# Kernel tuning notes

Hardware: AMD Instinct MI355X
Metric: run time of the kernel (lower is better)

The kernel has to match this reference:

```python
import jax, jax.numpy as jnp
import numpy as np

# index_map: new group -> list of old column indices (covers 23 old classes -> 10 groups)
INDEX_MAP = {0: [0, 1], 1: [2, 3], 2: [4, 5, 6], 3: [7, 8], 4: [9, 10, 11],
             5: [12, 13], 6: [14, 15, 16], 7: [17, 18], 8: [19, 20], 9: [21, 22]}
C_OLD = 23
G = len(INDEX_MAP)

# Membership matrix M[c, g] = 1 if old column c belongs to group g.
# outputs[:, g] = sum_{c in group g} inputs[:, c]  ==  inputs @ M
_M_np = np.zeros((C_OLD, G), dtype=np.float32)
for g, olds in INDEX_MAP.items():
    for c in olds:
        _M_np[c, g] = 1.0

B, N = 8, 262144


def setup_inputs() -> dict:
    key = jax.random.key(0)
    k1, k2 = jax.random.split(key)
    inputs = jax.random.uniform(k1, (B, N, C_OLD), dtype=jnp.float32)  # positive logits/scores
    t = jax.random.uniform(k2, (B, G), dtype=jnp.float32)
    targets = t / jnp.sum(t, axis=-1, keepdims=True)  # probability targets for KLDiv
    return {"inputs": inputs, "targets": targets}


def reference(inputs, targets):
    M = jnp.asarray(_M_np)                                 # [C, G]
    # grouped scatter-sum over columns (the nested loops in the original)
    outputs = jnp.einsum('bnc,cg->bng', inputs, M)         # [B, N, G]
    probs = outputs / jnp.sum(outputs, axis=-1, keepdims=True)
    avg_probs = jnp.mean(probs, axis=1)                    # [B, G]
    log_avg = jnp.log(avg_probs)
    # KLDivLoss(reduction='batchmean') on a 1-D input of length G divides by G:
    # loss_b = sum_g t[g] * (log t[g] - log_avg[g]) / G
    kl_per_b = jnp.sum(targets * (jnp.log(targets) - log_avg), axis=-1) / G
    return jnp.mean(kl_per_b)
```

## Files before the change

### kernel.cpp

```cpp
#include <hip/hip_runtime.h>
#include <math.h>

#define C_OLD 23
#define G 10
#define BVAL 8
#define NVAL 262144
#define ROWS_PER_BLOCK 256
#define BLOCK 256
#define TILE_FLOATS (ROWS_PER_BLOCK * C_OLD)
#define TILE_VEC4   (TILE_FLOATS / 4)
#define FULL_VEC_ITERS (TILE_VEC4 / BLOCK)

__global__ void zero_ws_kernel(double* acc) {
    int t = threadIdx.x;
    if (t < BVAL * G) acc[t] = 0.0;
}

__global__ __launch_bounds__(BLOCK) void group_prob_sum_kernel(
        const float* __restrict__ in, double* __restrict__ acc) {
    __shared__ float tile[TILE_FLOATS];
    __shared__ float wpart[BLOCK / 64][G];

    const int tid = threadIdx.x;
    const long long row0 = (long long)blockIdx.x * ROWS_PER_BLOCK;

    const float4* __restrict__ src = (const float4*)(in + row0 * C_OLD);
    float4* dst = (float4*)tile;
    #pragma unroll
    for (int i = 0; i < FULL_VEC_ITERS; ++i)
        dst[tid + i * BLOCK] = src[tid + i * BLOCK];
    {
        int rem = tid + FULL_VEC_ITERS * BLOCK;
        if (rem < TILE_VEC4) dst[rem] = src[rem];
    }
    __syncthreads();

    const float* row = tile + tid * C_OLD;
    float s0 = row[0] + row[1];
    float s1 = row[2] + row[3];
    float s2 = row[4] + row[5] + row[6];
    float s3 = row[7] + row[8];
    float s4 = row[9] + row[10] + row[11];
    float s5 = row[12] + row[13];
    float s6 = row[14] + row[15] + row[16];
    float s7 = row[17] + row[18];
    float s8 = row[19] + row[20];
    float s9 = row[21] + row[22];
    float tot = ((s0 + s1) + (s2 + s3)) + ((s4 + s5) + (s6 + s7)) + (s8 + s9);
    float inv = 1.0f / tot;

    float p[G];
    p[0] = s0 * inv; p[1] = s1 * inv; p[2] = s2 * inv; p[3] = s3 * inv;
    p[4] = s4 * inv; p[5] = s5 * inv; p[6] = s6 * inv; p[7] = s7 * inv;
    p[8] = s8 * inv; p[9] = s9 * inv;

    #pragma unroll
    for (int g = 0; g < G; ++g) {
        float v = p[g];
        #pragma unroll
        for (int off = 32; off > 0; off >>= 1)
            v += __shfl_down(v, off, 64);
        p[g] = v;
    }

    const int wave = tid >> 6;
    const int lane = tid & 63;
    if (lane == 0) {
        #pragma unroll
        for (int g = 0; g < G; ++g) wpart[wave][g] = p[g];
    }
    __syncthreads();

    if (tid < G) {
        float sum = wpart[0][tid] + wpart[1][tid] + wpart[2][tid] + wpart[3][tid];
        const int b = (int)(row0 >> 18);
        atomicAdd(&acc[b * G + tid], (double)sum);
    }
}

__global__ void finalize_kernel(const double* __restrict__ acc,
                                const float* __restrict__ tgt,
                                float* __restrict__ out) {
    __shared__ double red[128];
    const int t = threadIdx.x;
    double term = 0.0;
    if (t < BVAL * G) {
        double avg = acc[t] / (double)NVAL;
        double tv = (double)tgt[t];
        term = tv * (log(tv) - log(avg));
    }
    red[t] = term;
    __syncthreads();
    #pragma unroll
    for (int s = 64; s > 0; s >>= 1) {
        if (t < s) red[t] += red[t + s];
        __syncthreads();
    }
    if (t == 0) out[0] = (float)(red[0] / (double)(G * BVAL));
}

extern "C" void kernel_launch(void* const* d_in, const int* in_sizes, int n_in,
                              void* d_out, int out_size, void* d_ws, size_t ws_size,
                              hipStream_t stream) {
    const float* inputs  = (const float*)d_in[0];
    const float* targets = (const float*)d_in[1];
    float* out = (float*)d_out;
    double* acc = (double*)d_ws;

    zero_ws_kernel<<<1, 128, 0, stream>>>(acc);

    const long long total_rows = (long long)BVAL * NVAL;
    const int nblocks = (int)(total_rows / ROWS_PER_BLOCK);
    group_prob_sum_kernel<<<nblocks, BLOCK, 0, stream>>>(inputs, acc);

    finalize_kernel<<<1, 128, 0, stream>>>(acc, targets, out);
}
```

Baseline: 283.5 us.

## Process multiple tiles per block and replace double atomics with partial-sum buffer

Each block now loops over 8 tiles of 256 rows, accumulating group probabilities in registers, and launches 1024 blocks instead of 8192. It writes per-block partial sums to workspace and lets the finalize kernel reduce them, which removes the zero kernel and all double-precision atomics. The goal is to cut atomic contention and per-block reduction overhead. In exchange the grid is much smaller, so there is less latency hiding: each tile load is serialized behind a sync with no overlap between loading and compute.

Result: faster. 270.0 us (-4.8%).

```diff
diff --git a/kernel.cpp b/kernel.cpp
--- a/kernel.cpp
+++ b/kernel.cpp
@@ -5,88 +5,94 @@
 #define G 10
 #define BVAL 8
 #define NVAL 262144
-#define ROWS_PER_BLOCK 256
 #define BLOCK 256
-#define TILE_FLOATS (ROWS_PER_BLOCK * C_OLD)
+#define ROWS_PER_TILE 256
+#define TILES 8
+#define BLOCKS_PER_B 128
+#define TILE_FLOATS (ROWS_PER_TILE * C_OLD)
 #define TILE_VEC4   (TILE_FLOATS / 4)
 #define FULL_VEC_ITERS (TILE_VEC4 / BLOCK)
 
-__global__ void zero_ws_kernel(double* acc) {
-    int t = threadIdx.x;
-    if (t < BVAL * G) acc[t] = 0.0;
-}
-
-__global__ __launch_bounds__(BLOCK) void group_prob_sum_kernel(
-        const float* __restrict__ in, double* __restrict__ acc) {
+__global__ __launch_bounds__(BLOCK) void group_prob_partial_kernel(
+        const float* __restrict__ in, float* __restrict__ part) {
     __shared__ float tile[TILE_FLOATS];
     __shared__ float wpart[BLOCK / 64][G];
 
     const int tid = threadIdx.x;
-    const long long row0 = (long long)blockIdx.x * ROWS_PER_BLOCK;
+    const int b   = blockIdx.x / BLOCKS_PER_B;
+    const int blk = blockIdx.x % BLOCKS_PER_B;
+    const long long rowBase = (long long)b * NVAL
+                            + (long long)blk * (ROWS_PER_TILE * TILES);
 
-    const float4* __restrict__ src = (const float4*)(in + row0 * C_OLD);
-    float4* dst = (float4*)tile;
+    float acc[G];
     #pragma unroll
-    for (int i = 0; i < FULL_VEC_ITERS; ++i)
-        dst[tid + i * BLOCK] = src[tid + i * BLOCK];
-    {
-        int rem = tid + FULL_VEC_ITERS * BLOCK;
-        if (rem < TILE_VEC4) dst[rem] = src[rem];
+    for (int g = 0; g < G; ++g) acc[g] = 0.0f;
+
+    for (int t = 0; t < TILES; ++t) {
+        const float4* __restrict__ src =
+            (const float4*)(in + (rowBase + (long long)t * ROWS_PER_TILE) * C_OLD);
+        float4* dst = (float4*)tile;
+        #pragma unroll
+        for (int i = 0; i < FULL_VEC_ITERS; ++i)
+            dst[tid + i * BLOCK] = src[tid + i * BLOCK];
+        if (tid < TILE_VEC4 - FULL_VEC_ITERS * BLOCK)
+            dst[tid + FULL_VEC_ITERS * BLOCK] = src[tid + FULL_VEC_ITERS * BLOCK];
+        __syncthreads();
+
+        const float* row = tile + tid * C_OLD;
+        float s0 = row[0] + row[1];
+        float s1 = row[2] + row[3];
+        float s2 = row[4] + row[5] + row[6];
+        float s3 = row[7] + row[8];
+        float s4 = row[9] + row[10] + row[11];
+        float s5 = row[12] + row[13];
+        float s6 = row[14] + row[15] + row[16];
+        float s7 = row[17] + row[18];
+        float s8 = row[19] + row[20];
+        float s9 = row[21] + row[22];
+        float tot = ((s0 + s1) + (s2 + s3)) + ((s4 + s5) + (s6 + s7)) + (s8 + s9);
+        float inv = 1.0f / tot;
+        acc[0] += s0 * inv; acc[1] += s1 * inv; acc[2] += s2 * inv;
+        acc[3] += s3 * inv; acc[4] += s4 * inv; acc[5] += s5 * inv;
+        acc[6] += s6 * inv; acc[7] += s7 * inv; acc[8] += s8 * inv;
+        acc[9] += s9 * inv;
+        __syncthreads();
     }
-    __syncthreads();
-
-    const float* row = tile + tid * C_OLD;
-    float s0 = row[0] + row[1];
-    float s1 = row[2] + row[3];
-    float s2 = row[4] + row[5] + row[6];
-    float s3 = row[7] + row[8];
-    float s4 = row[9] + row[10] + row[11];
-    float s5 = row[12] + row[13];
-    float s6 = row[14] + row[15] + row[16];
-    float s7 = row[17] + row[18];
-    float s8 = row[19] + row[20];
-    float s9 = row[21] + row[22];
-    float tot = ((s0 + s1) + (s2 + s3)) + ((s4 + s5) + (s6 + s7)) + (s8 + s9);
-    float inv = 1.0f / tot;
-
-    float p[G];
-    p[0] = s0 * inv; p[1] = s1 * inv; p[2] = s2 * inv; p[3] = s3 * inv;
-    p[4] = s4 * inv; p[5] = s5 * inv; p[6] = s6 * inv; p[7] = s7 * inv;
-    p[8] = s8 * inv; p[9] = s9 * inv;
 
     #pragma unroll
     for (int g = 0; g < G; ++g) {
-        float v = p[g];
+        float v = acc[g];
         #pragma unroll
         for (int off = 32; off > 0; off >>= 1)
             v += __shfl_down(v, off, 64);
-        p[g] = v;
+        acc[g] = v;
     }
-
     const int wave = tid >> 6;
     const int lane = tid & 63;
     if (lane == 0) {
         #pragma unroll
-        for (int g = 0; g < G; ++g) wpart[wave][g] = p[g];
+        for (int g = 0; g < G; ++g) wpart[wave][g] = acc[g];
     }
     __syncthreads();
-
     if (tid < G) {
-        float sum = wpart[0][tid] + wpart[1][tid] + wpart[2][tid] + wpart[3][tid];
-        const int b = (int)(row0 >> 18);
-        atomicAdd(&acc[b * G + tid], (double)sum);
+        float s = wpart[0][tid] + wpart[1][tid] + wpart[2][tid] + wpart[3][tid];
+        part[((long long)b * G + tid) * BLOCKS_PER_B + blk] = s;
     }
 }
 
-__global__ void finalize_kernel(const double* __restrict__ acc,
+__global__ void finalize_kernel(const float* __restrict__ part,
                                 const float* __restrict__ tgt,
                                 float* __restrict__ out) {
     __shared__ double red[128];
     const int t = threadIdx.x;
     double term = 0.0;
     if (t < BVAL * G) {
-        double avg = acc[t] / (double)NVAL;
-        double tv = (double)tgt[t];
+        double s = 0.0;
+        const float* p = part + (long long)t * BLOCKS_PER_B;
+        #pragma unroll 8
+        for (int i = 0; i < BLOCKS_PER_B; ++i) s += (double)p[i];
+        double avg = s / (double)NVAL;
+        double tv  = (double)tgt[t];
         term = tv * (log(tv) - log(avg));
     }
     red[t] = term;
@@ -104,14 +110,9 @@
                               hipStream_t stream) {
     const float* inputs  = (const float*)d_in[0];
     const float* targets = (const float*)d_in[1];
-    float* out = (float*)d_out;
-    double* acc = (double*)d_ws;
+    float* out  = (float*)d_out;
+    float* part = (float*)d_ws;
 
-    zero_ws_kernel<<<1, 128, 0, stream>>>(acc);
-
-    const long long total_rows = (long long)BVAL * NVAL;
-    const int nblocks = (int)(total_rows / ROWS_PER_BLOCK);
-    group_prob_sum_kernel<<<nblocks, BLOCK, 0, stream>>>(inputs, acc);
-
-    finalize_kernel<<<1, 128, 0, stream>>>(acc, targets, out);
+    group_prob_partial_kernel<<<BVAL * BLOCKS_PER_B, BLOCK, 0, stream>>>(inputs, part);
+    finalize_kernel<<<1, 128, 0, stream>>>(part, targets, out);
 }
```
